# Performance work log

Measured on AMD Instinct MI355X. Metric: run time of the kernel, lower is better.

Reference implementation:

```python
import jax, jax.numpy as jnp
import numpy as np

N, D, H, E, TOP_K = 4096, 1024, 4096, 8, 2


def setup_inputs() -> dict:
    key = jax.random.key(0)
    ks = jax.random.split(key, 5)
    s_in = 1.0 / np.sqrt(D)
    s_hid = 1.0 / np.sqrt(H)
    return {
        "x": jax.random.normal(ks[0], (N, D), jnp.float32),
        "Wg": jax.random.normal(ks[1], (D, E), jnp.float32) * s_in,
        "bg": jnp.zeros((E,), jnp.float32),
        "W1": jax.random.normal(ks[2], (E, D, H), jnp.float32) * s_in,
        "b1": jnp.zeros((E, H), jnp.float32),
        "W2": jax.random.normal(ks[3], (E, H, D), jnp.float32) * s_hid,
        "b2": jnp.zeros((E, D), jnp.float32),
    }


def reference(x, Wg, bg, W1, b1, W2, b2):
    # Gating: softmax over experts, then top-k selection (weights NOT renormalized,
    # matching the original which multiplies raw topk softmax values).
    gate_scores = jax.nn.softmax(x @ Wg + bg, axis=-1)            # [N, E]
    topk_vals, topk_idx = jax.lax.top_k(gate_scores, TOP_K)       # [N, k]

    # Dense per-token combine weights: w[n, e] = sum of topk_vals where topk_idx == e
    n_ar = jnp.arange(x.shape[0])[:, None]
    w = jnp.zeros_like(gate_scores).at[n_ar, topk_idx].add(topk_vals)  # [N, E]

    # Expert FFN for every expert (dense grouped-GEMM form), weighted combine.
    h = jax.nn.relu(jnp.einsum('nd,edh->neh', x, W1) + b1)        # [N, E, H]
    y = jnp.einsum('neh,ehd->ned', h, W2) + b2                    # [N, E, D]
    return jnp.einsum('ne,ned->nd', w, y)                         # [N, D]
```

## Files before the change

### kernel.cpp

```cpp
#include <hip/hip_runtime.h>
#include <hip/hip_bf16.h>
#include <stdint.h>

#define NT 4096
#define DD 1024
#define HH 4096
#define NEXP 8

typedef __attribute__((ext_vector_type(8))) short bf16x8;
typedef __attribute__((ext_vector_type(4))) float f32x4;

#define GLOAD16(g, l) __builtin_amdgcn_global_load_lds( \
    (const __attribute__((address_space(1))) void*)(g), \
    (__attribute__((address_space(3))) void*)(l), 16, 0, 0)

__device__ inline ushort f2b(float f) {
  union { float f; uint32_t u; } v; v.f = f;
  uint32_t u = v.u;
  return (ushort)((u + 0x7fffu + ((u >> 16) & 1u)) >> 16);
}

__global__ __launch_bounds__(256) void gating_kernel(
    const float* __restrict__ x, const float* __restrict__ Wg,
    const float* __restrict__ bg, float* __restrict__ wgt,
    int* __restrict__ tidx, float* __restrict__ tval, int* __restrict__ counts) {
  int gw = (blockIdx.x * 256 + threadIdx.x) >> 6;
  int lane = threadIdx.x & 63;
  if (gw >= NT) return;
  const float* xr = x + (size_t)gw * DD;
  float acc[NEXP];
#pragma unroll
  for (int e = 0; e < NEXP; e++) acc[e] = 0.f;
  for (int d = lane; d < DD; d += 64) {
    float xv = xr[d];
    const float* wr = Wg + (size_t)d * NEXP;
#pragma unroll
    for (int e = 0; e < NEXP; e++) acc[e] += xv * wr[e];
  }
#pragma unroll
  for (int off = 32; off > 0; off >>= 1) {
#pragma unroll
    for (int e = 0; e < NEXP; e++) acc[e] += __shfl_xor(acc[e], off, 64);
  }
  float l[NEXP], m = -1e30f;
#pragma unroll
  for (int e = 0; e < NEXP; e++) { l[e] = acc[e] + bg[e]; m = fmaxf(m, l[e]); }
  float s = 0.f;
#pragma unroll
  for (int e = 0; e < NEXP; e++) { l[e] = expf(l[e] - m); s += l[e]; }
  float inv = 1.f / s;
  float v1 = -1.f, v2 = -1.f; int i1 = -1, i2 = -1;
#pragma unroll
  for (int e = 0; e < NEXP; e++) {
    float p = l[e] * inv;
    if (p > v1) { v2 = v1; i2 = i1; v1 = p; i1 = e; }
    else if (p > v2) { v2 = p; i2 = e; }
  }
  if (lane < NEXP) {
    float w = (lane == i1) ? v1 : ((lane == i2) ? v2 : 0.f);
    wgt[(size_t)gw * NEXP + lane] = w;
  }
  if (lane == 0) {
    tidx[gw * 2 + 0] = i1; tval[gw * 2 + 0] = v1;
    tidx[gw * 2 + 1] = i2; tval[gw * 2 + 1] = v2;
    atomicAdd(&counts[i1], 1);
    atomicAdd(&counts[i2], 1);
  }
}

__global__ void scan_kernel(const int* __restrict__ counts, int* __restrict__ base) {
  int b = 0;
#pragma unroll
  for (int e = 0; e < NEXP; e++) { base[e] = b; b += ((counts[e] + 127) >> 7) << 7; }
}

__global__ __launch_bounds__(256) void scatter_kernel(
    const int* __restrict__ tidx, const float* __restrict__ tval,
    const int* __restrict__ base, int* __restrict__ cursor,
    int* __restrict__ perm, float* __restrict__ pairw) {
  int t = blockIdx.x * 256 + threadIdx.x;
  if (t >= NT) return;
#pragma unroll
  for (int k = 0; k < 2; k++) {
    int e = tidx[t * 2 + k];
    int pos = atomicAdd(&cursor[e], 1);
    int p = base[e] + pos;
    perm[p] = t;
    pairw[p] = tval[t * 2 + k];
  }
}

__global__ __launch_bounds__(256) void cvt_x_kernel(
    const float* __restrict__ in, ushort* __restrict__ out, int n) {
  int i = (blockIdx.x * 256 + threadIdx.x) * 4;
  if (i >= n) return;
  float4 v = *(const float4*)(in + i);
  ushort4 o; o.x = f2b(v.x); o.y = f2b(v.y); o.z = f2b(v.z); o.w = f2b(v.w);
  *(ushort4*)(out + i) = o;
}

__global__ __launch_bounds__(256) void transpose_cvt_kernel(
    const float* __restrict__ in, ushort* __restrict__ out, int R, int C) {
  __shared__ float t[32][33];
  size_t eo = (size_t)blockIdx.z * R * C;
  in += eo; out += eo;
  int c0 = blockIdx.x * 32, r0 = blockIdx.y * 32;
  int tx = threadIdx.x & 31, ty = threadIdx.x >> 5;
#pragma unroll
  for (int i = 0; i < 4; i++) {
    int r = ty + i * 8;
    t[r][tx] = in[(size_t)(r0 + r) * C + c0 + tx];
  }
  __syncthreads();
#pragma unroll
  for (int i = 0; i < 4; i++) {
    int cc = ty + i * 8;
    out[(size_t)(c0 + cc) * R + r0 + tx] = f2b(t[tx][cc]);
  }
}

template <int MODE, bool SPARSE>
__global__ __launch_bounds__(256) void gemm_bt_kernel(
    const ushort* __restrict__ A, const ushort* __restrict__ BtAll,
    const float* __restrict__ biasAll, void* __restrict__ Cout,
    const int* __restrict__ perm, const float* __restrict__ pairw,
    const float* __restrict__ wgtDense,
    const int* __restrict__ base, const int* __restrict__ cnt,
    int Nn, int K, int eFixed) {
  const int BK = 32;
  __shared__ __align__(16) ushort As[128 * BK];
  __shared__ __align__(16) ushort Bs[128 * BK];
  int e, m0;
  if (SPARSE) {
    e = blockIdx.z;
    if ((int)blockIdx.y * 128 >= cnt[e]) return;
    m0 = base[e] + blockIdx.y * 128;
  } else {
    e = eFixed;
    m0 = blockIdx.y * 128;
  }
  int n0 = blockIdx.x * 128;
  const ushort* Bt = SPARSE ? BtAll + (size_t)e * Nn * K : BtAll;
  const float* bias = biasAll + (size_t)e * Nn;

  int tid = threadIdx.x, wv = tid >> 6, lane = tid & 63;
  int sr = lane >> 2;
  int sc = (lane & 3) * 8;
  int ar0 = m0 + wv * 32 + sr, ar1 = ar0 + 16;
  int64_t gr0, gr1;
  if (SPARSE && MODE == 1) { gr0 = perm[ar0]; gr1 = perm[ar1]; }
  else { gr0 = ar0; gr1 = ar1; }
  const ushort* gA0 = A + gr0 * (int64_t)K + sc;
  const ushort* gA1 = A + gr1 * (int64_t)K + sc;
  const ushort* gB0 = Bt + (int64_t)(n0 + wv * 32 + sr) * K + sc;
  const ushort* gB1 = gB0 + (int64_t)16 * K;
  ushort* lA0 = &As[(wv * 32) * BK];
  ushort* lA1 = &As[(wv * 32 + 16) * BK];
  ushort* lB0 = &Bs[(wv * 32) * BK];
  ushort* lB1 = &Bs[(wv * 32 + 16) * BK];

  int wr = (wv >> 1) * 64;
  int wc = (wv & 1) * 64;
  int lr = lane & 15;
  int kq = (lane >> 4) * 8;

  f32x4 acc[4][4];
#pragma unroll
  for (int i = 0; i < 4; i++)
#pragma unroll
    for (int j = 0; j < 4; j++) acc[i][j] = (f32x4)(0.f);

  for (int k0 = 0; k0 < K; k0 += BK) {
    __syncthreads();
    GLOAD16(gA0 + k0, lA0);
    GLOAD16(gA1 + k0, lA1);
    GLOAD16(gB0 + k0, lB0);
    GLOAD16(gB1 + k0, lB1);
    __syncthreads();
    bf16x8 af[4], bfr[4];
#pragma unroll
    for (int i = 0; i < 4; i++)
      af[i] = *(const bf16x8*)&As[(wr + i * 16 + lr) * BK + kq];
#pragma unroll
    for (int j = 0; j < 4; j++)
      bfr[j] = *(const bf16x8*)&Bs[(wc + j * 16 + lr) * BK + kq];
#pragma unroll
    for (int i = 0; i < 4; i++)
#pragma unroll
      for (int j = 0; j < 4; j++)
        acc[i][j] = __builtin_amdgcn_mfma_f32_16x16x32_bf16(af[i], bfr[j],
                                                            acc[i][j], 0, 0, 0);
  }

  int rq = (lane >> 4) * 4;
  if (MODE == 1) {
    ushort* Cb = (ushort*)Cout;
#pragma unroll
    for (int i = 0; i < 4; i++) {
#pragma unroll
      for (int r = 0; r < 4; r++) {
        int row = m0 + wr + i * 16 + rq + r;
#pragma unroll
        for (int j = 0; j < 4; j++) {
          int col = n0 + wc + j * 16 + lr;
          float v = acc[i][j][r] + bias[col];
          Cb[(size_t)row * Nn + col] = f2b(fmaxf(v, 0.f));
        }
      }
    }
  } else {
    float* Co = (float*)Cout;
#pragma unroll
    for (int i = 0; i < 4; i++) {
#pragma unroll
      for (int r = 0; r < 4; r++) {
        int row = m0 + wr + i * 16 + rq + r;
        if (SPARSE) {
          float w = pairw[row];
          if (w != 0.f) {
            int t = perm[row];
#pragma unroll
            for (int j = 0; j < 4; j++) {
              int col = n0 + wc + j * 16 + lr;
              atomicAdd(&Co[(size_t)t * DD + col], w * (acc[i][j][r] + bias[col]));
            }
          }
        } else {
          float w = wgtDense[(size_t)row * NEXP + e];
          if (w != 0.f) {
#pragma unroll
            for (int j = 0; j < 4; j++) {
              int col = n0 + wc + j * 16 + lr;
              Co[(size_t)row * Nn + col] += w * (acc[i][j][r] + bias[col]);
            }
          }
        }
      }
    }
  }
}

extern "C" void kernel_launch(void* const* d_in, const int* in_sizes, int n_in,
                              void* d_out, int out_size, void* d_ws,
                              size_t ws_size, hipStream_t stream) {
  const float* x  = (const float*)d_in[0];
  const float* Wg = (const float*)d_in[1];
  const float* bg = (const float*)d_in[2];
  const float* W1 = (const float*)d_in[3];
  const float* b1 = (const float*)d_in[4];
  const float* W2 = (const float*)d_in[5];
  const float* b2 = (const float*)d_in[6];
  float* out = (float*)d_out;
  char* ws = (char*)d_ws;

  hipMemsetAsync(d_out, 0, (size_t)out_size * sizeof(float), stream);

  const size_t XB_SZ   = (size_t)NT * DD * 2;
  const size_t WT_SZ   = (size_t)NEXP * DD * HH * 2;
  const size_t HB_ROWS = 9216;
  const size_t HB_SZ   = HB_ROWS * HH * 2;
  const size_t W1T_OFF = XB_SZ;
  const size_t W2T_OFF = W1T_OFF + WT_SZ;
  const size_t HB_OFF  = W2T_OFF + WT_SZ;
  const size_t SM_OFF  = HB_OFF + HB_SZ;
  const size_t TIER_A_NEED = SM_OFF + 275456;

  if (ws_size >= TIER_A_NEED) {
    ushort* xb   = (ushort*)ws;
    ushort* w1t  = (ushort*)(ws + W1T_OFF);
    ushort* w2t  = (ushort*)(ws + W2T_OFF);
    ushort* hbuf = (ushort*)(ws + HB_OFF);
    char* sm = ws + SM_OFF;
    int*   counts = (int*)(sm + 0);
    int*   cursor = (int*)(sm + 128);
    int*   base   = (int*)(sm + 256);
    int*   tidx   = (int*)(sm + 1024);
    float* tval   = (float*)(sm + 1024 + 32768);
    int*   perm   = (int*)(sm + 68608);
    float* pairw  = (float*)(sm + 105472);
    float* wgt    = (float*)(sm + 143360);

    hipMemsetAsync(sm, 0, 142336, stream);

    gating_kernel<<<NT / 4, 256, 0, stream>>>(x, Wg, bg, wgt, tidx, tval, counts);
    cvt_x_kernel<<<(NT * DD / 4 + 255) / 256, 256, 0, stream>>>(x, xb, NT * DD);
    scan_kernel<<<1, 1, 0, stream>>>(counts, base);
    scatter_kernel<<<NT / 256, 256, 0, stream>>>(tidx, tval, base, cursor, perm, pairw);

    transpose_cvt_kernel<<<dim3(HH / 32, DD / 32, NEXP), 256, 0, stream>>>(W1, w1t, DD, HH);
    transpose_cvt_kernel<<<dim3(DD / 32, HH / 32, NEXP), 256, 0, stream>>>(W2, w2t, HH, DD);

    gemm_bt_kernel<1, true><<<dim3(HH / 128, NT / 128, NEXP), 256, 0, stream>>>(
        xb, w1t, b1, hbuf, perm, pairw, nullptr, base, counts, HH, DD, 0);
    gemm_bt_kernel<2, true><<<dim3(DD / 128, NT / 128, NEXP), 256, 0, stream>>>(
        hbuf, w2t, b2, out, perm, pairw, nullptr, base, counts, DD, HH, 0);
    return;
  }

  ushort* xb  = (ushort*)ws;
  ushort* hb  = (ushort*)(ws + (8u << 20));
  ushort* w1t = (ushort*)(ws + (42u << 20));
  ushort* w2t = (ushort*)(ws + (51u << 20));
  char* sm2 = ws + (59u << 20);
  int*   tidx   = (int*)(sm2);
  float* tval   = (float*)(sm2 + 32768);
  int*   counts = (int*)(sm2 + 65536);
  float* wgt    = (float*)(ws + (60u << 20));

  gating_kernel<<<NT / 4, 256, 0, stream>>>(x, Wg, bg, wgt, tidx, tval, counts);
  cvt_x_kernel<<<(NT * DD / 4 + 255) / 256, 256, 0, stream>>>(x, xb, NT * DD);

  for (int e = 0; e < NEXP; e++) {
    transpose_cvt_kernel<<<dim3(HH / 32, DD / 32, 1), 256, 0, stream>>>(
        W1 + (size_t)e * DD * HH, w1t, DD, HH);
    gemm_bt_kernel<1, false><<<dim3(HH / 128, NT / 128, 1), 256, 0, stream>>>(
        xb, w1t, b1, hb, nullptr, nullptr, nullptr, nullptr, nullptr, HH, DD, e);
    transpose_cvt_kernel<<<dim3(DD / 32, HH / 32, 1), 256, 0, stream>>>(
        W2 + (size_t)e * HH * DD, w2t, HH, DD);
    gemm_bt_kernel<2, false><<<dim3(DD / 128, NT / 128, 1), 256, 0, stream>>>(
        hb, w2t, b2, out, nullptr, nullptr, wgt, nullptr, nullptr, DD, HH, e);
  }
}
```

Before: 797.2 us.

## Vectorize weight transpose-convert and split-K the second expert GEMM

The weight transpose-convert kernel now uses 64x64 tiles, converts to bf16 before staging in swizzled shared memory, and does float4 loads with 16-byte stores, to cut memory traffic and instruction count in the weight preprocessing. The second sparse GEMM is split four ways along K across extra grid blocks, and each split atomically accumulates into the output, with bias added only by the first split. This raises parallelism for the down-projection, whose output-tile grid is small. The cost is four times as many atomic adds to the output.

```diff
diff --git a/kernel.cpp b/kernel.cpp
--- a/kernel.cpp
+++ b/kernel.cpp
@@ -99,27 +99,42 @@
   *(ushort4*)(out + i) = o;
 }
 
-__global__ __launch_bounds__(256) void transpose_cvt_kernel(
+__global__ __launch_bounds__(256) void transpose_cvt64_kernel(
     const float* __restrict__ in, ushort* __restrict__ out, int R, int C) {
-  __shared__ float t[32][33];
-  size_t eo = (size_t)blockIdx.z * R * C;
+  __shared__ __align__(16) ushort T[64 * 68];
+  size_t eo = (size_t)blockIdx.z * (size_t)R * C;
   in += eo; out += eo;
-  int c0 = blockIdx.x * 32, r0 = blockIdx.y * 32;
-  int tx = threadIdx.x & 31, ty = threadIdx.x >> 5;
+  int r0 = blockIdx.y * 64, c0 = blockIdx.x * 64;
+  int t = threadIdx.x;
+  int lr = t >> 4;
+  int lc = (t & 15) * 4;
 #pragma unroll
   for (int i = 0; i < 4; i++) {
-    int r = ty + i * 8;
-    t[r][tx] = in[(size_t)(r0 + r) * C + c0 + tx];
+    int r = lr + i * 16;
+    float4 v = *(const float4*)(in + (size_t)(r0 + r) * C + c0 + lc);
+    ushort4 o; o.x = f2b(v.x); o.y = f2b(v.y); o.z = f2b(v.z); o.w = f2b(v.w);
+    int cs = lc ^ (((r >> 3) & 7) << 3);
+    *(ushort4*)&T[r * 68 + cs] = o;
   }
   __syncthreads();
 #pragma unroll
-  for (int i = 0; i < 4; i++) {
-    int cc = ty + i * 8;
-    out[(size_t)(c0 + cc) * R + r0 + tx] = f2b(t[tx][cc]);
-  }
-}
-
-template <int MODE, bool SPARSE>
+  for (int it = 0; it < 2; it++) {
+    int task = it * 256 + t;
+    int c = task >> 3;
+    int rr0 = (task & 7) * 8;
+    uint w[4];
+#pragma unroll
+    for (int j = 0; j < 4; j++) {
+      int ra = rr0 + 2 * j, rb = ra + 1;
+      uint a = T[ra * 68 + (c ^ (((ra >> 3) & 7) << 3))];
+      uint b = T[rb * 68 + (c ^ (((rb >> 3) & 7) << 3))];
+      w[j] = a | (b << 16);
+    }
+    *(uint4*)(out + (size_t)(c0 + c) * R + r0 + rr0) = make_uint4(w[0], w[1], w[2], w[3]);
+  }
+}
+
+template <int MODE, bool SPARSE, int SPLITS>
 __global__ __launch_bounds__(256) void gemm_bt_kernel(
     const ushort* __restrict__ A, const ushort* __restrict__ BtAll,
     const float* __restrict__ biasAll, void* __restrict__ Cout,
@@ -130,13 +145,14 @@
   const int BK = 32;
   __shared__ __align__(16) ushort As[128 * BK];
   __shared__ __align__(16) ushort Bs[128 * BK];
-  int e, m0;
+  int e, sp, m0;
   if (SPARSE) {
-    e = blockIdx.z;
+    e = blockIdx.z / SPLITS;
+    sp = blockIdx.z % SPLITS;
     if ((int)blockIdx.y * 128 >= cnt[e]) return;
     m0 = base[e] + blockIdx.y * 128;
   } else {
-    e = eFixed;
+    e = eFixed; sp = 0;
     m0 = blockIdx.y * 128;
   }
   int n0 = blockIdx.x * 128;
@@ -170,7 +186,8 @@
 #pragma unroll
     for (int j = 0; j < 4; j++) acc[i][j] = (f32x4)(0.f);
 
-  for (int k0 = 0; k0 < K; k0 += BK) {
+  int kb = (K / SPLITS) * sp, ke = kb + K / SPLITS;
+  for (int k0 = kb; k0 < ke; k0 += BK) {
     __syncthreads();
     GLOAD16(gA0 + k0, lA0);
     GLOAD16(gA1 + k0, lA1);
@@ -222,7 +239,8 @@
 #pragma unroll
             for (int j = 0; j < 4; j++) {
               int col = n0 + wc + j * 16 + lr;
-              atomicAdd(&Co[(size_t)t * DD + col], w * (acc[i][j][r] + bias[col]));
+              float bterm = (sp == 0) ? bias[col] : 0.f;
+              atomicAdd(&Co[(size_t)t * DD + col], w * (acc[i][j][r] + bterm));
             }
           }
         } else {
@@ -287,12 +305,12 @@
     scan_kernel<<<1, 1, 0, stream>>>(counts, base);
     scatter_kernel<<<NT / 256, 256, 0, stream>>>(tidx, tval, base, cursor, perm, pairw);
 
-    transpose_cvt_kernel<<<dim3(HH / 32, DD / 32, NEXP), 256, 0, stream>>>(W1, w1t, DD, HH);
-    transpose_cvt_kernel<<<dim3(DD / 32, HH / 32, NEXP), 256, 0, stream>>>(W2, w2t, HH, DD);
-
-    gemm_bt_kernel<1, true><<<dim3(HH / 128, NT / 128, NEXP), 256, 0, stream>>>(
+    transpose_cvt64_kernel<<<dim3(HH / 64, DD / 64, NEXP), 256, 0, stream>>>(W1, w1t, DD, HH);
+    transpose_cvt64_kernel<<<dim3(DD / 64, HH / 64, NEXP), 256, 0, stream>>>(W2, w2t, HH, DD);
+
+    gemm_bt_kernel<1, true, 1><<<dim3(HH / 128, NT / 128, NEXP), 256, 0, stream>>>(
         xb, w1t, b1, hbuf, perm, pairw, nullptr, base, counts, HH, DD, 0);
-    gemm_bt_kernel<2, true><<<dim3(DD / 128, NT / 128, NEXP), 256, 0, stream>>>(
+    gemm_bt_kernel<2, true, 4><<<dim3(DD / 128, NT / 128, NEXP * 4), 256, 0, stream>>>(
         hbuf, w2t, b2, out, perm, pairw, nullptr, base, counts, DD, HH, 0);
     return;
   }
@@ -311,13 +329,13 @@
   cvt_x_kernel<<<(NT * DD / 4 + 255) / 256, 256, 0, stream>>>(x, xb, NT * DD);
 
   for (int e = 0; e < NEXP; e++) {
-    transpose_cvt_kernel<<<dim3(HH / 32, DD / 32, 1), 256, 0, stream>>>(
+    transpose_cvt64_kernel<<<dim3(HH / 64, DD / 64, 1), 256, 0, stream>>>(
         W1 + (size_t)e * DD * HH, w1t, DD, HH);
-    gemm_bt_kernel<1, false><<<dim3(HH / 128, NT / 128, 1), 256, 0, stream>>>(
+    gemm_bt_kernel<1, false, 1><<<dim3(HH / 128, NT / 128, 1), 256, 0, stream>>>(
         xb, w1t, b1, hb, nullptr, nullptr, nullptr, nullptr, nullptr, HH, DD, e);
-    transpose_cvt_kernel<<<dim3(DD / 32, HH / 32, 1), 256, 0, stream>>>(
+    transpose_cvt64_kernel<<<dim3(DD / 64, HH / 64, 1), 256, 0, stream>>>(
         W2 + (size_t)e * HH * DD, w2t, HH, DD);
-    gemm_bt_kernel<2, false><<<dim3(DD / 128, NT / 128, 1), 256, 0, stream>>>(
+    gemm_bt_kernel<2, false, 1><<<dim3(DD / 128, NT / 128, 1), 256, 0, stream>>>(
         hb, w2t, b2, out, nullptr, nullptr, wgt, nullptr, nullptr, DD, HH, e);
   }
 }
```

Result: slower. 865.3 us (+8.6%).
